# Performance work log

Measured on AMD Instinct MI355X. Metric: run time of the kernel, lower is better.

Reference implementation:

```python
import jax, jax.numpy as jnp
import numpy as np

B, S, E, H, MAXLEN = 2, 2048, 1024, 16, 2048


def _level_indices(seq_len: int, base: int = 2) -> np.ndarray:
    """Vectorized version of get_level_index_weak over the full (target, source) grid.
    indices[t, s] = min(level, 2) for s < t, else 0. Runs in O(log S) passes."""
    tt = np.broadcast_to(np.arange(seq_len)[:, None], (seq_len, seq_len)).astype(np.int64).copy()
    ss = np.broadcast_to(np.arange(seq_len)[None, :], (seq_len, seq_len)).astype(np.int64).copy()
    res = np.zeros((seq_len, seq_len), np.int64)
    done = ~(ss < tt)  # only source < target positions get a level; rest stay 0
    while not done.all():
        l = np.floor(np.log2(np.maximum(tt, 1).astype(np.float64))).astype(np.int64)
        v = (np.int64(1) << l)
        hit = (~done) & (ss < v)
        res[hit] = l[hit] + 1
        done |= hit
        step = ~done
        tt[step] -= v[step]
        ss[step] -= v[step]
    return np.minimum(res, 2).astype(np.int32)


def setup_inputs() -> dict:
    key = jax.random.key(0)
    ks = jax.random.split(key, 10)
    sc = 0.02
    return {
        "x": jax.random.normal(ks[0], (B, S, E), dtype=jnp.float32),
        "attention_mask": jax.random.randint(ks[1], (B, S), 0, 2, dtype=jnp.int32),
        "level_indices": jnp.asarray(_level_indices(S, 2)),
        "Wq": jax.random.normal(ks[2], (E, E), dtype=jnp.float32) * sc,
        "bq": jnp.zeros((E,), jnp.float32),
        "Wk": jax.random.normal(ks[3], (E, E), dtype=jnp.float32) * sc,
        "bk": jnp.zeros((E,), jnp.float32),
        "Wv": jax.random.normal(ks[4], (E, E), dtype=jnp.float32) * sc,
        "bv": jnp.zeros((E,), jnp.float32),
        "hier": jax.random.normal(ks[5], (MAXLEN, H, 3), dtype=jnp.float32),
        "Wo": jax.random.normal(ks[6], (E, E), dtype=jnp.float32) * sc,
        "bo": jnp.zeros((E,), jnp.float32),
    }


def reference(x, attention_mask, level_indices, Wq, bq, Wk, bk, Wv, bv, hier, Wo, bo):
    b, s, e = x.shape
    h = hier.shape[1]
    dh = e // h
    # q/k are computed by the original module but never used; kept for fidelity (zero grads).
    q = x @ Wq.T + bq
    k = x @ Wk.T + bk
    v = (x @ Wv.T + bv).reshape(b, s, h, dh).transpose(0, 2, 1, 3)  # [B,H,S,Dh]
    lev = level_indices[:s, :s]  # [S,S] int, values in {0,1,2}
    # Faithful torch.gather semantics: weights[b,h,i,j] = hier[b, h, lev[i,j]]
    w3 = hier[:b]                      # [B,H,3]
    weights = w3[:, :, lev]            # [B,H,S,S]
    decay = jnp.power(jnp.float32(0.5), lev.astype(x.dtype))  # [S,S]
    weights = weights * decay
    weights = weights / (jnp.sum(weights, axis=-1, keepdims=True) + 1e-8)
    weights = jnp.where(attention_mask[:, None, None, :] == 0, jnp.float32(0.0), weights)
    out = jnp.einsum('bhij,bhjd->bhid', weights, v)  # [B,H,S,Dh]
    out = out.transpose(0, 2, 1, 3).reshape(b, s, e)
    return out @ Wo.T + bo
```

## Files before the change

### kernel.cpp

```cpp
#include <hip/hip_runtime.h>
#include <cstdint>
#include <cstddef>

constexpr int Sn = 2048;
constexpr int En = 1024;
constexpr int Bn = 2;
constexpr int Hn = 16;
constexpr int NCH = 32;
constexpr int CHUNK = 64;

typedef __bf16 bf16x8 __attribute__((ext_vector_type(8)));
typedef float  f32x4  __attribute__((ext_vector_type(4)));

#define GLOBAL_AS(p) ((const __attribute__((address_space(1))) void*)(p))
#define LDS_AS(p)    ((__attribute__((address_space(3))) void*)(p))

__device__ __forceinline__ unsigned short f2bf(float f) {
    union { float f; uint32_t u; } v; v.f = f;
    const uint32_t u = v.u;
    return (unsigned short)((u + 0x7fffu + ((u >> 16) & 1u)) >> 16);
}

__global__ __launch_bounds__(256)
void cast_bf16(const float* __restrict__ src, unsigned short* __restrict__ dst, int n)
{
    const int i = (blockIdx.x * 256 + threadIdx.x) * 4;
    if (i >= n) return;
    const float4 v = *(const float4*)(src + i);
    ushort4 o;
    o.x = f2bf(v.x); o.y = f2bf(v.y); o.z = f2bf(v.z); o.w = f2bf(v.w);
    *(ushort4*)(dst + i) = o;
}

template<bool APPLY_MASK>
__global__ __launch_bounds__(256)
void gemm_mfma(const unsigned short* __restrict__ A, const unsigned short* __restrict__ Bw,
               const float* __restrict__ bias, const int* __restrict__ mask,
               float* __restrict__ C, int M, int N, int K)
{
    __shared__ __align__(16) unsigned short As[128 * 32];
    __shared__ __align__(16) unsigned short Bs[128 * 32];

    const int tid  = threadIdx.x;
    const int lane = tid & 63;
    const int wv   = tid >> 6;
    const int wr   = wv >> 1;
    const int wc   = wv & 1;
    const int bm   = blockIdx.y * 128;
    const int bn   = blockIdx.x * 128;
    const int m16  = lane & 15;
    const int kq   = lane >> 4;

    f32x4 acc[4][4] = {};

    const int j0 = 2 * wv, j1 = 2 * wv + 1;
    const unsigned short* gA0 = A  + (size_t)(bm + 16 * j0 + m16) * K + kq * 8;
    const unsigned short* gA1 = A  + (size_t)(bm + 16 * j1 + m16) * K + kq * 8;
    const unsigned short* gB0 = Bw + (size_t)(bn + 16 * j0 + m16) * K + kq * 8;
    const unsigned short* gB1 = Bw + (size_t)(bn + 16 * j1 + m16) * K + kq * 8;
    unsigned short* lA0 = &As[j0 * 512];
    unsigned short* lA1 = &As[j1 * 512];
    unsigned short* lB0 = &Bs[j0 * 512];
    unsigned short* lB1 = &Bs[j1 * 512];

    for (int k0 = 0; k0 < K; k0 += 32) {
        __syncthreads();
        __builtin_amdgcn_global_load_lds(GLOBAL_AS(gA0 + k0), LDS_AS(lA0), 16, 0, 0);
        __builtin_amdgcn_global_load_lds(GLOBAL_AS(gA1 + k0), LDS_AS(lA1), 16, 0, 0);
        __builtin_amdgcn_global_load_lds(GLOBAL_AS(gB0 + k0), LDS_AS(lB0), 16, 0, 0);
        __builtin_amdgcn_global_load_lds(GLOBAL_AS(gB1 + k0), LDS_AS(lB1), 16, 0, 0);
        __syncthreads();

        bf16x8 af[4], bfr[4];
#pragma unroll
        for (int i = 0; i < 4; ++i)
            af[i] = *(const bf16x8*)&As[(wr * 4 + i) * 512 + lane * 8];
#pragma unroll
        for (int j = 0; j < 4; ++j)
            bfr[j] = *(const bf16x8*)&Bs[(wc * 4 + j) * 512 + lane * 8];
#pragma unroll
        for (int i = 0; i < 4; ++i)
#pragma unroll
            for (int j = 0; j < 4; ++j)
                acc[i][j] = __builtin_amdgcn_mfma_f32_16x16x32_bf16(af[i], bfr[j], acc[i][j], 0, 0, 0);
    }

#pragma unroll
    for (int i = 0; i < 4; ++i) {
        const int r0 = bm + wr * 64 + i * 16 + kq * 4;
#pragma unroll
        for (int j = 0; j < 4; ++j) {
            const int c0 = bn + wc * 64 + j * 16 + m16;
            const float bcol = bias[c0];
#pragma unroll
            for (int r = 0; r < 4; ++r) {
                const int row = r0 + r;
                float val = acc[i][j][r] + bcol;
                if (APPLY_MASK) val = (mask[row] == 0) ? 0.0f : val;
                C[(size_t)row * N + c0] = val;
            }
        }
    }
}

__global__ __launch_bounds__(256)
void chunk_sum(const float* __restrict__ vm, float* __restrict__ csum)
{
    const int e = blockIdx.x * 256 + threadIdx.x;
    const int c = blockIdx.y;
    const int b = blockIdx.z;
    const size_t base = ((size_t)b * Sn + c * CHUNK) * En + e;
    float s = 0.0f;
    for (int t = 0; t < CHUNK; ++t) s += vm[base + (size_t)t * En];
    csum[((size_t)b * NCH + c) * En + e] = s;
}

__global__ __launch_bounds__(256)
void chunk_scan(const float* __restrict__ csum, float* __restrict__ cscan,
                float* __restrict__ Tbuf)
{
    const int idx = blockIdx.x * 256 + threadIdx.x;
    const int b = idx >> 10;
    const int e = idx & (En - 1);
    float run = 0.0f;
    for (int c = 0; c < NCH; ++c) {
        const size_t off = ((size_t)b * NCH + c) * En + e;
        const float v = csum[off];
        cscan[off] = run;
        run += v;
    }
    Tbuf[idx] = run;
}

__global__ __launch_bounds__(256)
void combine(const float* __restrict__ vm, const float* __restrict__ cscan,
             const float* __restrict__ Tbuf, const float* __restrict__ hier,
             unsigned short* __restrict__ opre)
{
    const int e = blockIdx.x * 256 + threadIdx.x;
    const int c = blockIdx.y;
    const int b = blockIdx.z;
    const int h = e >> 6;

    const float w0 = hier[((size_t)b * Hn + h) * 3 + 0];
    const float w1 = hier[((size_t)b * Hn + h) * 3 + 1] * 0.5f;
    const float w2 = hier[((size_t)b * Hn + h) * 3 + 2] * 0.25f;
    const float T  = Tbuf[(size_t)b * En + e];

    float run  = cscan[((size_t)b * NCH + c) * En + e];
    float prev = 0.0f;
    const size_t base = ((size_t)b * Sn + c * CHUNK) * En + e;

    for (int t = 0; t < CHUNK; ++t) {
        const int i = c * CHUNK + t;
        const float cur = vm[base + (size_t)t * En];
        float num, Z;
        if (i & 1) {
            const float pm = run - prev;
            num = w2 * pm + w1 * prev + w0 * (T - run);
            Z = (float)(i - 1) * w2 + w1 + (float)(Sn - i) * w0 + 1e-8f;
        } else {
            num = w2 * run + w0 * (T - run);
            Z = (float)i * w2 + (float)(Sn - i) * w0 + 1e-8f;
        }
        opre[base + (size_t)t * En] = f2bf(num / Z);
        run  += cur;
        prev  = cur;
    }
}

extern "C" void kernel_launch(void* const* d_in, const int* in_sizes, int n_in,
                              void* d_out, int out_size, void* d_ws, size_t ws_size,
                              hipStream_t stream)
{
    const float* x    = (const float*)d_in[0];
    const int*   mask = (const int*)d_in[1];
    const float* Wv   = (const float*)d_in[7];
    const float* bv   = (const float*)d_in[8];
    const float* hier = (const float*)d_in[9];
    const float* Wo   = (const float*)d_in[10];
    const float* bo   = (const float*)d_in[11];
    float* out = (float*)d_out;

    const int M = Bn * Sn, N = En, K = En;

    char* ws = (char*)d_ws;
    unsigned short* xb    = (unsigned short*)ws;                ws += (size_t)M * K * 2;
    unsigned short* Wvb   = (unsigned short*)ws;                ws += (size_t)N * K * 2;
    unsigned short* Wob   = (unsigned short*)ws;                ws += (size_t)N * K * 2;
    float*          vm    = (float*)ws;                         ws += (size_t)M * N * 4;
    float*          csum  = (float*)ws;                         ws += (size_t)Bn * NCH * En * 4;
    float*          cscan = (float*)ws;                         ws += (size_t)Bn * NCH * En * 4;
    float*          Tbuf  = (float*)ws;                         ws += (size_t)Bn * En * 4;
    unsigned short* opreb = (unsigned short*)ws;                ws += (size_t)M * N * 2;

    dim3 threads(256);

    cast_bf16<<<dim3((M * K) / 1024), threads, 0, stream>>>(x,  xb,  M * K);
    cast_bf16<<<dim3((N * K) / 1024), threads, 0, stream>>>(Wv, Wvb, N * K);
    cast_bf16<<<dim3((N * K) / 1024), threads, 0, stream>>>(Wo, Wob, N * K);

    dim3 gemm_grid(N / 128, M / 128);

    gemm_mfma<true><<<gemm_grid, threads, 0, stream>>>(xb, Wvb, bv, mask, vm, M, N, K);
    chunk_sum<<<dim3(En / 256, NCH, Bn), threads, 0, stream>>>(vm, csum);
    chunk_scan<<<dim3((Bn * En) / 256), threads, 0, stream>>>(csum, cscan, Tbuf);
    combine<<<dim3(En / 256, NCH, Bn), threads, 0, stream>>>(vm, cscan, Tbuf, hier, opreb);
    gemm_mfma<false><<<gemm_grid, threads, 0, stream>>>(opreb, Wob, bo, nullptr, out, M, N, K);
}
```

Baseline: 200.4 us.

## Fuse casts, halve GEMM N-tile, store V in bf16, vectorize scan kernels

Merges the three fp32-to-bf16 cast launches into one kernel and shrinks the GEMM block tile from 128x128 to 128x64, doubling the grid to 512 blocks for better CU occupancy on 4096x1024 GEMMs. The V projection is written as bf16 instead of fp32, halving traffic for the chunk_sum and combine passes, which now process two columns per thread with packed 32-bit loads and stores. Combine also replaces the per-element divide with a reciprocal multiply. The smaller tile lowers data reuse per block, and storing V in bf16 adds rounding before the prefix sums.

After: 177.8 us. 1.13x faster.

```diff
diff --git a/kernel.cpp b/kernel.cpp
--- a/kernel.cpp
+++ b/kernel.cpp
@@ -20,26 +20,40 @@
     const uint32_t u = v.u;
     return (unsigned short)((u + 0x7fffu + ((u >> 16) & 1u)) >> 16);
 }
-
-__global__ __launch_bounds__(256)
-void cast_bf16(const float* __restrict__ src, unsigned short* __restrict__ dst, int n)
+__device__ __forceinline__ float bf2f_lo(uint32_t u) {
+    union { uint32_t u; float f; } v; v.u = u << 16; return v.f;
+}
+__device__ __forceinline__ float bf2f_hi(uint32_t u) {
+    union { uint32_t u; float f; } v; v.u = u & 0xffff0000u; return v.f;
+}
+
+constexpr int XN = Bn * Sn * En;
+constexpr int WN = En * En;
+
+__global__ __launch_bounds__(256)
+void cast3(const float* __restrict__ x, const float* __restrict__ Wv,
+           const float* __restrict__ Wo, unsigned short* __restrict__ xb,
+           unsigned short* __restrict__ Wvb, unsigned short* __restrict__ Wob)
 {
     const int i = (blockIdx.x * 256 + threadIdx.x) * 4;
-    if (i >= n) return;
-    const float4 v = *(const float4*)(src + i);
+    const float* src; unsigned short* dst; int off;
+    if (i < XN)           { src = x;  dst = xb;  off = i; }
+    else if (i < XN + WN) { src = Wv; dst = Wvb; off = i - XN; }
+    else                  { src = Wo; dst = Wob; off = i - XN - WN; }
+    const float4 v = *(const float4*)(src + off);
     ushort4 o;
     o.x = f2bf(v.x); o.y = f2bf(v.y); o.z = f2bf(v.z); o.w = f2bf(v.w);
-    *(ushort4*)(dst + i) = o;
-}
-
-template<bool APPLY_MASK>
+    *(ushort4*)(dst + off) = o;
+}
+
+template<bool APPLY_MASK, bool OUT_BF16>
 __global__ __launch_bounds__(256)
 void gemm_mfma(const unsigned short* __restrict__ A, const unsigned short* __restrict__ Bw,
                const float* __restrict__ bias, const int* __restrict__ mask,
-               float* __restrict__ C, int M, int N, int K)
+               void* __restrict__ Cv, int M, int N, int K)
 {
     __shared__ __align__(16) unsigned short As[128 * 32];
-    __shared__ __align__(16) unsigned short Bs[128 * 32];
+    __shared__ __align__(16) unsigned short Bs[64 * 32];
 
     const int tid  = threadIdx.x;
     const int lane = tid & 63;
@@ -47,41 +61,38 @@
     const int wr   = wv >> 1;
     const int wc   = wv & 1;
     const int bm   = blockIdx.y * 128;
-    const int bn   = blockIdx.x * 128;
+    const int bn   = blockIdx.x * 64;
     const int m16  = lane & 15;
     const int kq   = lane >> 4;
 
-    f32x4 acc[4][4] = {};
+    f32x4 acc[4][2] = {};
 
     const int j0 = 2 * wv, j1 = 2 * wv + 1;
     const unsigned short* gA0 = A  + (size_t)(bm + 16 * j0 + m16) * K + kq * 8;
     const unsigned short* gA1 = A  + (size_t)(bm + 16 * j1 + m16) * K + kq * 8;
-    const unsigned short* gB0 = Bw + (size_t)(bn + 16 * j0 + m16) * K + kq * 8;
-    const unsigned short* gB1 = Bw + (size_t)(bn + 16 * j1 + m16) * K + kq * 8;
+    const unsigned short* gB0 = Bw + (size_t)(bn + 16 * wv + m16) * K + kq * 8;
     unsigned short* lA0 = &As[j0 * 512];
     unsigned short* lA1 = &As[j1 * 512];
-    unsigned short* lB0 = &Bs[j0 * 512];
-    unsigned short* lB1 = &Bs[j1 * 512];
+    unsigned short* lB0 = &Bs[wv * 512];
 
     for (int k0 = 0; k0 < K; k0 += 32) {
         __syncthreads();
         __builtin_amdgcn_global_load_lds(GLOBAL_AS(gA0 + k0), LDS_AS(lA0), 16, 0, 0);
         __builtin_amdgcn_global_load_lds(GLOBAL_AS(gA1 + k0), LDS_AS(lA1), 16, 0, 0);
         __builtin_amdgcn_global_load_lds(GLOBAL_AS(gB0 + k0), LDS_AS(lB0), 16, 0, 0);
-        __builtin_amdgcn_global_load_lds(GLOBAL_AS(gB1 + k0), LDS_AS(lB1), 16, 0, 0);
         __syncthreads();
 
-        bf16x8 af[4], bfr[4];
+        bf16x8 af[4], bfr[2];
 #pragma unroll
         for (int i = 0; i < 4; ++i)
             af[i] = *(const bf16x8*)&As[(wr * 4 + i) * 512 + lane * 8];
 #pragma unroll
-        for (int j = 0; j < 4; ++j)
-            bfr[j] = *(const bf16x8*)&Bs[(wc * 4 + j) * 512 + lane * 8];
+        for (int j = 0; j < 2; ++j)
+            bfr[j] = *(const bf16x8*)&Bs[(wc * 2 + j) * 512 + lane * 8];
 #pragma unroll
         for (int i = 0; i < 4; ++i)
 #pragma unroll
-            for (int j = 0; j < 4; ++j)
+            for (int j = 0; j < 2; ++j)
                 acc[i][j] = __builtin_amdgcn_mfma_f32_16x16x32_bf16(af[i], bfr[j], acc[i][j], 0, 0, 0);
     }
 
@@ -89,30 +100,40 @@
     for (int i = 0; i < 4; ++i) {
         const int r0 = bm + wr * 64 + i * 16 + kq * 4;
 #pragma unroll
-        for (int j = 0; j < 4; ++j) {
-            const int c0 = bn + wc * 64 + j * 16 + m16;
+        for (int j = 0; j < 2; ++j) {
+            const int c0 = bn + wc * 32 + j * 16 + m16;
             const float bcol = bias[c0];
 #pragma unroll
             for (int r = 0; r < 4; ++r) {
                 const int row = r0 + r;
                 float val = acc[i][j][r] + bcol;
                 if (APPLY_MASK) val = (mask[row] == 0) ? 0.0f : val;
-                C[(size_t)row * N + c0] = val;
+                if (OUT_BF16)
+                    ((unsigned short*)Cv)[(size_t)row * N + c0] = f2bf(val);
+                else
+                    ((float*)Cv)[(size_t)row * N + c0] = val;
             }
         }
     }
 }
 
 __global__ __launch_bounds__(256)
-void chunk_sum(const float* __restrict__ vm, float* __restrict__ csum)
-{
-    const int e = blockIdx.x * 256 + threadIdx.x;
+void chunk_sum(const unsigned short* __restrict__ vm, float* __restrict__ csum)
+{
+    const int ep = blockIdx.x * 256 + threadIdx.x;
+    const int e = ep * 2;
     const int c = blockIdx.y;
     const int b = blockIdx.z;
     const size_t base = ((size_t)b * Sn + c * CHUNK) * En + e;
-    float s = 0.0f;
-    for (int t = 0; t < CHUNK; ++t) s += vm[base + (size_t)t * En];
-    csum[((size_t)b * NCH + c) * En + e] = s;
+    float s0 = 0.0f, s1 = 0.0f;
+    for (int t = 0; t < CHUNK; ++t) {
+        const uint32_t u = *(const uint32_t*)(vm + base + (size_t)t * En);
+        s0 += bf2f_lo(u);
+        s1 += bf2f_hi(u);
+    }
+    const size_t o = ((size_t)b * NCH + c) * En + e;
+    csum[o] = s0;
+    csum[o + 1] = s1;
 }
 
 __global__ __launch_bounds__(256)
@@ -133,11 +154,12 @@
 }
 
 __global__ __launch_bounds__(256)
-void combine(const float* __restrict__ vm, const float* __restrict__ cscan,
+void combine(const unsigned short* __restrict__ vm, const float* __restrict__ cscan,
              const float* __restrict__ Tbuf, const float* __restrict__ hier,
              unsigned short* __restrict__ opre)
 {
-    const int e = blockIdx.x * 256 + threadIdx.x;
+    const int ep = blockIdx.x * 256 + threadIdx.x;
+    const int e = ep * 2;
     const int c = blockIdx.y;
     const int b = blockIdx.z;
     const int h = e >> 6;
@@ -145,27 +167,33 @@
     const float w0 = hier[((size_t)b * Hn + h) * 3 + 0];
     const float w1 = hier[((size_t)b * Hn + h) * 3 + 1] * 0.5f;
     const float w2 = hier[((size_t)b * Hn + h) * 3 + 2] * 0.25f;
-    const float T  = Tbuf[(size_t)b * En + e];
-
-    float run  = cscan[((size_t)b * NCH + c) * En + e];
-    float prev = 0.0f;
+    const float T0 = Tbuf[(size_t)b * En + e];
+    const float T1 = Tbuf[(size_t)b * En + e + 1];
+
+    const size_t co = ((size_t)b * NCH + c) * En + e;
+    float run0 = cscan[co], run1 = cscan[co + 1];
+    float prev0 = 0.0f, prev1 = 0.0f;
     const size_t base = ((size_t)b * Sn + c * CHUNK) * En + e;
 
     for (int t = 0; t < CHUNK; ++t) {
         const int i = c * CHUNK + t;
-        const float cur = vm[base + (size_t)t * En];
-        float num, Z;
+        const uint32_t u = *(const uint32_t*)(vm + base + (size_t)t * En);
+        const float cur0 = bf2f_lo(u), cur1 = bf2f_hi(u);
+        float num0, num1, Z;
         if (i & 1) {
-            const float pm = run - prev;
-            num = w2 * pm + w1 * prev + w0 * (T - run);
+            num0 = w2 * (run0 - prev0) + w1 * prev0 + w0 * (T0 - run0);
+            num1 = w2 * (run1 - prev1) + w1 * prev1 + w0 * (T1 - run1);
             Z = (float)(i - 1) * w2 + w1 + (float)(Sn - i) * w0 + 1e-8f;
         } else {
-            num = w2 * run + w0 * (T - run);
+            num0 = w2 * run0 + w0 * (T0 - run0);
+            num1 = w2 * run1 + w0 * (T1 - run1);
             Z = (float)i * w2 + (float)(Sn - i) * w0 + 1e-8f;
         }
-        opre[base + (size_t)t * En] = f2bf(num / Z);
-        run  += cur;
-        prev  = cur;
+        const float rz = 1.0f / Z;
+        const uint32_t o = (uint32_t)f2bf(num0 * rz) | ((uint32_t)f2bf(num1 * rz) << 16);
+        *(uint32_t*)(opre + base + (size_t)t * En) = o;
+        run0 += cur0; run1 += cur1;
+        prev0 = cur0; prev1 = cur1;
     }
 }
 
@@ -185,26 +213,24 @@
     const int M = Bn * Sn, N = En, K = En;
 
     char* ws = (char*)d_ws;
-    unsigned short* xb    = (unsigned short*)ws;                ws += (size_t)M * K * 2;
-    unsigned short* Wvb   = (unsigned short*)ws;                ws += (size_t)N * K * 2;
-    unsigned short* Wob   = (unsigned short*)ws;                ws += (size_t)N * K * 2;
-    float*          vm    = (float*)ws;                         ws += (size_t)M * N * 4;
-    float*          csum  = (float*)ws;                         ws += (size_t)Bn * NCH * En * 4;
-    float*          cscan = (float*)ws;                         ws += (size_t)Bn * NCH * En * 4;
-    float*          Tbuf  = (float*)ws;                         ws += (size_t)Bn * En * 4;
-    unsigned short* opreb = (unsigned short*)ws;                ws += (size_t)M * N * 2;
+    unsigned short* xb    = (unsigned short*)ws;  ws += (size_t)M * K * 2;
+    unsigned short* Wvb   = (unsigned short*)ws;  ws += (size_t)N * K * 2;
+    unsigned short* Wob   = (unsigned short*)ws;  ws += (size_t)N * K * 2;
+    unsigned short* vmb   = (unsigned short*)ws;  ws += (size_t)M * N * 2;
+    float*          csum  = (float*)ws;           ws += (size_t)Bn * NCH * En * 4;
+    float*          cscan = (float*)ws;           ws += (size_t)Bn * NCH * En * 4;
+    float*          Tbuf  = (float*)ws;           ws += (size_t)Bn * En * 4;
+    unsigned short* opreb = (unsigned short*)ws;  ws += (size_t)M * N * 2;
 
     dim3 threads(256);
 
-    cast_bf16<<<dim3((M * K) / 1024), threads, 0, stream>>>(x,  xb,  M * K);
-    cast_bf16<<<dim3((N * K) / 1024), threads, 0, stream>>>(Wv, Wvb, N * K);
-    cast_bf16<<<dim3((N * K) / 1024), threads, 0, stream>>>(Wo, Wob, N * K);
-
-    dim3 gemm_grid(N / 128, M / 128);
-
-    gemm_mfma<true><<<gemm_grid, threads, 0, stream>>>(xb, Wvb, bv, mask, vm, M, N, K);
-    chunk_sum<<<dim3(En / 256, NCH, Bn), threads, 0, stream>>>(vm, csum);
+    cast3<<<dim3((XN + 2 * WN) / 1024), threads, 0, stream>>>(x, Wv, Wo, xb, Wvb, Wob);
+
+    dim3 gemm_grid(N / 64, M / 128);
+
+    gemm_mfma<true, true><<<gemm_grid, threads, 0, stream>>>(xb, Wvb, bv, mask, vmb, M, N, K);
+    chunk_sum<<<dim3(En / 512, NCH, Bn), threads, 0, stream>>>(vmb, csum);
     chunk_scan<<<dim3((Bn * En) / 256), threads, 0, stream>>>(csum, cscan, Tbuf);
-    combine<<<dim3(En / 256, NCH, Bn), threads, 0, stream>>>(vm, cscan, Tbuf, hier, opreb);
-    gemm_mfma<false><<<gemm_grid, threads, 0, stream>>>(opreb, Wob, bo, nullptr, out, M, N, K);
-}
+    combine<<<dim3(En / 512, NCH, Bn), threads, 0, stream>>>(vmb, cscan, Tbuf, hier, opreb);
+    gemm_mfma<false, false><<<gemm_grid, threads, 0, stream>>>(opreb, Wob, bo, nullptr, out, M, N, K);
+}
```
